# Optimization experiments

Hardware: AMD Instinct MI355X
Metric: run time of the kernel (lower is better)

## Reference

```python
import jax, jax.numpy as jnp
import numpy as np

HID = 64   # basis_hidden_dim
NB = 8     # num_learnable_bases
N = 16     # n_super_nodes
D = 4      # latent_dim
B = 2048   # batch

_PNAMES = ["W1", "b1", "W2", "b2", "W3", "b3", "scale", "aW1", "ab1", "aW2", "ab2", "res"]


def _basis_params(key, din):
    ks = jax.random.split(key, 4)
    s = 0.1
    return [
        jax.random.normal(ks[0], (NB, din, HID)) * s, jnp.zeros((NB, HID)),
        jax.random.normal(ks[1], (NB, HID, HID)) * s, jnp.zeros((NB, HID)),
        jax.random.normal(ks[2], (NB, HID, 1)) * s, jnp.zeros((NB, 1)),
        jnp.ones((NB,)),
        jax.random.normal(ks[3], (din, HID // 2)) * s, jnp.zeros((HID // 2,)),
        jax.random.normal(jax.random.fold_in(ks[3], 1), (HID // 2, NB)) * s, jnp.zeros((NB,)),
        jnp.ones((1,)) * 0.1,
    ]


def setup_inputs() -> dict:
    key = jax.random.key(0)
    k0, k1, k2, k3, k4 = jax.random.split(key, 5)
    inp = {"z_flat": jax.random.normal(k0, (B, N * D), dtype=jnp.float32)}
    for pfx, kk, din in [("pw", k1, 8), ("nd", k2, D), ("gl", k3, N * D)]:
        for nm, v in zip(_PNAMES, _basis_params(kk, din)):
            inp[pfx + "_" + nm] = v
    ks = jax.random.split(k4, 3)
    inp["sel_W1"] = jax.random.normal(ks[0], (N * D, HID)) * 0.1
    inp["sel_b1"] = jnp.zeros((HID,))
    inp["sel_W2"] = jax.random.normal(ks[1], (HID, HID // 2)) * 0.1
    inp["sel_b2"] = jnp.zeros((HID // 2,))
    inp["sel_W3"] = jax.random.normal(ks[2], (HID // 2, 1)) * 0.1
    inp["sel_b3"] = jnp.zeros((1,))
    return inp


def _basis(x, W1, b1, W2, b2, W3, b3, scale, aW1, ab1, aW2, ab2, res):
    # x: [..., din] -> [..., 1]. NB tiny 3-layer MLPs batched over basis axis n.
    h = jax.nn.silu(jnp.einsum('...i,nih->...nh', x, W1) + b1)
    h = jax.nn.silu(jnp.einsum('...nh,nhk->...nk', h, W2) + b2)
    o = (jnp.einsum('...nh,nh->...n', h, W3[..., 0]) + b3[:, 0]) * scale  # [..., NB]
    # attention mixing over the NB basis outputs
    a = jax.nn.silu(x @ aW1 + ab1)
    a = jax.nn.softmax(a @ aW2 + ab2, axis=-1)                            # [..., NB]
    out = jnp.sum(o * a, axis=-1, keepdims=True)
    return out + res * jnp.mean(x, axis=-1, keepdims=True)                # residual


def _forward(z_flat,
             pw_W1, pw_b1, pw_W2, pw_b2, pw_W3, pw_b3, pw_scale, pw_aW1, pw_ab1, pw_aW2, pw_ab2, pw_res,
             nd_W1, nd_b1, nd_W2, nd_b2, nd_W3, nd_b3, nd_scale, nd_aW1, nd_ab1, nd_aW2, nd_ab2, nd_res,
             gl_W1, gl_b1, gl_W2, gl_b2, gl_W3, gl_b3, gl_scale, gl_aW1, gl_ab1, gl_aW2, gl_ab2, gl_res,
             sel_W1, sel_b1, sel_W2, sel_b2, sel_W3, sel_b3):
    b = z_flat.shape[0]
    z_nodes = z_flat.reshape(b, N, D)
    pos = z_nodes[:, :, :2]
    iu, ju = jnp.triu_indices(N, k=1)  # P = N*(N-1)/2 = 120 pairs
    # pairwise distances on upper-triangular pairs (no box wrap: box_size=None)
    diffs = pos[:, iu] - pos[:, ju]                     # [B, P, 2]
    d = jnp.sqrt(jnp.sum(diffs * diffs, axis=-1))       # [B, P]
    d = jnp.maximum(d, 0.001)
    inv_d = 1.0 / (d + 0.1)
    inv_sq = 1.0 / (d * d + 0.1)
    exp_d = jnp.exp(-jnp.minimum(d, 20.0))
    screened = exp_d / (d + 0.1)
    log_d = jnp.log(d + 1.0)
    # learnable pairwise basis: cat(pos_i, vel_i, pos_j, vel_j) == cat(z_i, z_j) for D=4
    pair_in = jnp.concatenate([z_nodes[:, iu], z_nodes[:, ju]], axis=-1)  # [B, P, 8]
    pw = _basis(pair_in, pw_W1, pw_b1, pw_W2, pw_b2, pw_W3, pw_b3, pw_scale,
                pw_aW1, pw_ab1, pw_aW2, pw_ab2, pw_res)[..., 0]           # [B, P]
    nd = _basis(z_nodes, nd_W1, nd_b1, nd_W2, nd_b2, nd_W3, nd_b3, nd_scale,
                nd_aW1, nd_ab1, nd_aW2, nd_ab2, nd_res)[..., 0]           # [B, N]
    gl = _basis(z_flat, gl_W1, gl_b1, gl_W2, gl_b2, gl_W3, gl_b3, gl_scale,
                gl_aW1, gl_ab1, gl_aW2, gl_ab2, gl_res)                   # [B, 1]
    X = jnp.concatenate([z_flat, d, inv_d, inv_sq, exp_d, screened, log_d, pw, nd, gl], axis=1)
    # adaptive feature selection gate
    s = jax.nn.silu(z_flat @ sel_W1 + sel_b1)
    s = jax.nn.silu(s @ sel_W2 + sel_b2)
    s = jax.nn.sigmoid(s @ sel_W3 + sel_b3)             # [B, 1]
    X = X * s
    return jnp.clip(X, -1e6, 1e6)


def reference(z_flat,
              pw_W1, pw_b1, pw_W2, pw_b2, pw_W3, pw_b3, pw_scale, pw_aW1, pw_ab1, pw_aW2, pw_ab2, pw_res,
              nd_W1, nd_b1, nd_W2, nd_b2, nd_W3, nd_b3, nd_scale, nd_aW1, nd_ab1, nd_aW2, nd_ab2, nd_res,
              gl_W1, gl_b1, gl_W2, gl_b2, gl_W3, gl_b3, gl_scale, gl_aW1, gl_ab1, gl_aW2, gl_ab2, gl_res,
              sel_W1, sel_b1, sel_W2, sel_b2, sel_W3, sel_b3):
    return _forward(z_flat,
                    pw_W1, pw_b1, pw_W2, pw_b2, pw_W3, pw_b3, pw_scale, pw_aW1, pw_ab1, pw_aW2, pw_ab2, pw_res,
                    nd_W1, nd_b1, nd_W2, nd_b2, nd_W3, nd_b3, nd_scale, nd_aW1, nd_ab1, nd_aW2, nd_ab2, nd_res,
                    gl_W1, gl_b1, gl_W2, gl_b2, gl_W3, gl_b3, gl_scale, gl_aW1, gl_ab1, gl_aW2, gl_ab2, gl_res,
                    sel_W1, sel_b1, sel_W2, sel_b2, sel_W3, sel_b3)
```

## Files before the change

kernel.cpp:

```cpp
#include <hip/hip_runtime.h>
#include <hip/hip_bf16.h>
#include <math.h>

#define XCOLS 921
#define COL_Z 0
#define COL_D 64
#define COL_INVD 184
#define COL_INVSQ 304
#define COL_EXPD 424
#define COL_SCR 544
#define COL_LOGD 664
#define COL_PW 784
#define COL_ND 904
#define COL_GL 920

#define BATCH 2048
#define NPAIRS 120
#define RPW (BATCH * NPAIRS)
#define RND (BATCH * 16)
#define RGL BATCH
#define RTOT (RPW + RND + RGL)

#define ROWS_BLK 128
#define TILES 8
#define GL_BLK 16
#define PW_BLK 1920
#define ND_BLK 256

#define PREP_SG   512
#define PREP_ROW  1096
#define PREP_WP   128

#define WS_SGATE   0u
#define WS_ZERO    8192u
#define WS_ONE     8448u
#define WS_BW3_PW  8704u
#define WS_BW3_ND  12800u
#define WS_BW3_GL  16896u
#define WS_B1D_GL  20992u
#define WS_W1T_PW  23040u
#define WS_W1T_ND  39424u
#define WS_W1T_GL  55808u
#define WS_W2T_PW  121344u
#define WS_W2T_ND  186880u
#define WS_W2T_GL  252416u
#define WS_XF      317952u
#define WS_XGL     4774400u
#define WS_ATT     5036544u
#define WS_TAIL    14014976u

typedef unsigned short ushort_t;
typedef unsigned int uint_t;
typedef __attribute__((ext_vector_type(8))) short bf16x8;
typedef __attribute__((ext_vector_type(4))) float f32x4;

__device__ __forceinline__ float fast_rcp(float x) { return __builtin_amdgcn_rcpf(x); }
__device__ __forceinline__ float silu_f(float x) { return x * fast_rcp(1.0f + __expf(-x)); }
__device__ __forceinline__ ushort_t f2b(float f) {
    __hip_bfloat16 h = __float2bfloat16(f);
    return __builtin_bit_cast(ushort_t, h);
}
__device__ __forceinline__ uint_t pk2(float a, float b) {
    return (uint_t)f2b(a) | ((uint_t)f2b(b) << 16);
}
__device__ __forceinline__ int permS(int m) {
    return ((m >> 2) & 3) * 8 + (m & 3) + ((m >> 4) & 1) * 4 + ((m >> 5) & 1) * 32;
}

struct AArgs { const float *aW1, *ab1, *aW2, *ab2, *b3, *scale, *res; };
struct PArgs { const float *W1, *b1, *W2, *b2, *W3; };
struct SArgs { const float *W1, *b1, *W2, *b2, *W3, *b3; };

__global__ __launch_bounds__(256) void prep_all_kernel(
    const float* __restrict__ z,
    SArgs sel,
    AArgs apw, AArgs anda, AArgs agl,
    PArgs ppw, PArgs pnd, PArgs pgl,
    char* __restrict__ ws, float* __restrict__ out)
{
    const int bid = blockIdx.x;
    const int tid = threadIdx.x;

    if (bid < PREP_SG) {
        __shared__ float zs[4][64];
        __shared__ float h1[4][64];
        __shared__ float h2s[4][32];
        __shared__ float sgv[4];
        const int grp = tid >> 6, tl = tid & 63;
        const int b = bid * 4 + grp;
        zs[grp][tl] = z[b * 64 + tl];
        __syncthreads();
        {
            float acc = sel.b1[tl];
            #pragma unroll
            for (int i = 0; i < 64; ++i) acc += zs[grp][i] * sel.W1[i * 64 + tl];
            h1[grp][tl] = silu_f(acc);
        }
        __syncthreads();
        if (tl < 32) {
            float acc = sel.b2[tl];
            #pragma unroll
            for (int i = 0; i < 64; ++i) acc += h1[grp][i] * sel.W2[i * 32 + tl];
            h2s[grp][tl] = silu_f(acc);
        }
        __syncthreads();
        if (tl == 0) {
            float acc = sel.b3[0];
            #pragma unroll
            for (int i = 0; i < 32; ++i) acc += h2s[grp][i] * sel.W3[i];
            float s = fast_rcp(1.0f + __expf(-acc));
            sgv[grp] = s;
            ((float*)(ws + WS_SGATE))[b] = s;
        }
        __syncthreads();
        float s = sgv[grp];
        float* row = out + (size_t)b * XCOLS;
        {
            float v = zs[grp][tl] * s;
            row[COL_Z + tl] = fminf(fmaxf(v, -1e6f), 1e6f);
        }
        #pragma unroll
        for (int rep = 0; rep < 2; ++rep) {
            int p = tl + rep * 64;
            if (p < NPAIRS) {
                int i = 0, pp = p;
                while (pp >= 15 - i) { pp -= 15 - i; ++i; }
                int j = i + 1 + pp;
                float dx = zs[grp][i * 4 + 0] - zs[grp][j * 4 + 0];
                float dy = zs[grp][i * 4 + 1] - zs[grp][j * 4 + 1];
                float d = sqrtf(dx * dx + dy * dy);
                d = fmaxf(d, 0.001f);
                float inv_d = fast_rcp(d + 0.1f);
                float inv_sq = fast_rcp(d * d + 0.1f);
                float exp_d = __expf(-fminf(d, 20.0f));
                float screened = exp_d * inv_d;
                float log_d = __logf(d + 1.0f);
                row[COL_D + p] = d * s;
                row[COL_INVD + p] = inv_d * s;
                row[COL_INVSQ + p] = inv_sq * s;
                row[COL_EXPD + p] = exp_d * s;
                row[COL_SCR + p] = screened * s;
                row[COL_LOGD + p] = log_d * s;
            }
        }
        return;
    }

    if (bid >= PREP_SG + PREP_ROW) {
        int t0 = (bid - (PREP_SG + PREP_ROW)) * 256 + tid;
        const int STR = PREP_WP * 256;
        if (t0 < 64) ((float*)(ws + WS_ZERO))[t0] = 0.f;
        if (t0 < 8) ((ushort_t*)(ws + WS_ONE))[t0] = (t0 == 0) ? f2b(1.0f) : (ushort_t)0;
        for (int t = t0; t < 16384; t += STR) {
            int which = t >> 13, u = t & 8191;
            int nn = u >> 10, m = (u >> 4) & 63, k = u & 15;
            int sm = permS(m);
            float v;
            if (which == 0)
                v = (k < 8) ? ppw.W1[nn * 512 + k * 64 + sm]
                  : (k == 8 ? ppw.b1[nn * 64 + sm] : 0.f);
            else
                v = (k < 4) ? pnd.W1[nn * 256 + k * 64 + sm]
                  : (k == 8 ? pnd.b1[nn * 64 + sm] : 0.f);
            ((ushort_t*)(ws + (which == 0 ? WS_W1T_PW : WS_W1T_ND)))[u] = f2b(v);
        }
        for (int t = t0; t < 32768; t += STR) {
            int nn = t >> 12, m = (t >> 6) & 63, k = t & 63;
            ((ushort_t*)(ws + WS_W1T_GL))[t] = f2b(pgl.W1[nn * 4096 + k * 64 + permS(m)]);
        }
        for (int t = t0; t < 512; t += STR) {
            int nn = t >> 6, m = t & 63;
            ((float*)(ws + WS_B1D_GL))[t] = pgl.b1[nn * 64 + permS(m)];
        }
        for (int t = t0; t < 3 * 32768; t += STR) {
            int which = t >> 15, u = t & 32767;
            int nn = u >> 12, kb = (u >> 9) & 7, col = (u >> 3) & 63, e = u & 7;
            int k = (kb & 3) * 8 + e + ((kb >> 2) << 5);
            const float* src = which == 0 ? ppw.W2 : which == 1 ? pnd.W2 : pgl.W2;
            ushort_t* dst = (ushort_t*)(ws + (which == 0 ? WS_W2T_PW : which == 1 ? WS_W2T_ND : WS_W2T_GL));
            dst[u] = f2b(src[nn * 4096 + k * 64 + col]);
        }
        for (int t = t0; t < 1536; t += STR) {
            int which = t >> 9, u = t & 511;
            const float* b2 = which == 0 ? ppw.b2 : which == 1 ? pnd.b2 : pgl.b2;
            const float* W3 = which == 0 ? ppw.W3 : which == 1 ? pnd.W3 : pgl.W3;
            float2* dst = (float2*)(ws + (which == 0 ? WS_BW3_PW : which == 1 ? WS_BW3_ND : WS_BW3_GL));
            dst[u] = make_float2(b2[u], W3[u]);
        }
        return;
    }

    const int urow = (bid - PREP_SG) * 256 + tid;
    float a1acc[32];
    float mean;
    AArgs A;

    if (urow < RPW) {
        A = apw;
        int b = urow / 120, p = urow - b * 120;
        int i = 0, pp = p;
        while (pp >= 15 - i) { pp -= 15 - i; ++i; }
        int j = i + 1 + pp;
        const float* zb = z + b * 64;
        float4 xa = *(const float4*)(zb + i * 4);
        float4 xb = *(const float4*)(zb + j * 4);
        float x[8] = {xa.x, xa.y, xa.z, xa.w, xb.x, xb.y, xb.z, xb.w};
        uint4 xw = make_uint4(pk2(x[0], x[1]), pk2(x[2], x[3]), pk2(x[4], x[5]), pk2(x[6], x[7]));
        *(uint4*)(ws + WS_XF + (size_t)urow * 16) = xw;
        mean = (x[0] + x[1] + x[2] + x[3] + x[4] + x[5] + x[6] + x[7]) * 0.125f;
        #pragma unroll
        for (int u = 0; u < 32; ++u) {
            float acc = A.ab1[u];
            #pragma unroll
            for (int q = 0; q < 8; ++q) acc += x[q] * A.aW1[q * 32 + u];
            a1acc[u] = acc;
        }
    } else if (urow < RPW + RND) {
        A = anda;
        int loc = urow - RPW;
        int b = loc >> 4, node = loc & 15;
        float4 xa = *(const float4*)(z + b * 64 + node * 4);
        float x[4] = {xa.x, xa.y, xa.z, xa.w};
        uint4 xw = make_uint4(pk2(x[0], x[1]), pk2(x[2], x[3]), 0u, 0u);
        *(uint4*)(ws + WS_XF + (size_t)urow * 16) = xw;
        mean = (x[0] + x[1] + x[2] + x[3]) * 0.25f;
        #pragma unroll
        for (int u = 0; u < 32; ++u) {
            float acc = A.ab1[u];
            #pragma unroll
            for (int q = 0; q < 4; ++q) acc += x[q] * A.aW1[q * 32 + u];
            a1acc[u] = acc;
        }
    } else {
        A = agl;
        int r = urow - (RPW + RND);
        const float* zr = z + (size_t)r * 64;
        #pragma unroll
        for (int u = 0; u < 32; ++u) a1acc[u] = A.ab1[u];
        float mn = 0.f;
        #pragma unroll
        for (int c = 0; c < 8; ++c) {
            float4 f0 = *(const float4*)(zr + c * 8);
            float4 f1 = *(const float4*)(zr + c * 8 + 4);
            float xs[8] = {f0.x, f0.y, f0.z, f0.w, f1.x, f1.y, f1.z, f1.w};
            uint4 xw = make_uint4(pk2(xs[0], xs[1]), pk2(xs[2], xs[3]),
                                  pk2(xs[4], xs[5]), pk2(xs[6], xs[7]));
            *(uint4*)(ws + WS_XGL + (size_t)r * 128 + c * 16) = xw;
            #pragma unroll
            for (int q = 0; q < 8; ++q) {
                mn += xs[q];
                float xk = xs[q];
                #pragma unroll
                for (int u = 0; u < 32; ++u) a1acc[u] += xk * A.aW1[(c * 8 + q) * 32 + u];
            }
        }
        mean = mn * (1.0f / 64.0f);
    }

    float lg[8];
    #pragma unroll
    for (int n = 0; n < 8; ++n) lg[n] = A.ab2[n];
    #pragma unroll
    for (int u = 0; u < 32; ++u) {
        float a1 = silu_f(a1acc[u]);
        #pragma unroll
        for (int n = 0; n < 8; ++n) lg[n] += a1 * A.aW2[u * 8 + n];
    }
    float m = lg[0];
    #pragma unroll
    for (int n = 1; n < 8; ++n) m = fmaxf(m, lg[n]);
    float sum = 0.f;
    #pragma unroll
    for (int n = 0; n < 8; ++n) { lg[n] = __expf(lg[n] - m); sum += lg[n]; }
    float inv = fast_rcp(sum);
    float tail = 0.f;
    float as_[8];
    #pragma unroll
    for (int n = 0; n < 8; ++n) {
        float a_n = lg[n] * inv * A.scale[n];
        tail += a_n * A.b3[n];
        as_[n] = a_n;
    }
    float* ag = (float*)(ws + WS_ATT) + (size_t)urow * 8;
    *(float4*)(ag + 0) = make_float4(as_[0], as_[1], as_[2], as_[3]);
    *(float4*)(ag + 4) = make_float4(as_[4], as_[5], as_[6], as_[7]);
    ((float*)(ws + WS_TAIL))[urow] = tail + A.res[0] * mean;
}

__global__ __launch_bounds__(512, 4) void basis_main_kernel(
    const char* __restrict__ ws, float* __restrict__ out)
{
    __shared__ float Att[ROWS_BLK * 9];
    __shared__ float Part[8][ROWS_BLK];
    const int tid = threadIdx.x;
    const int lane = tid & 63;
    const int n = tid >> 6;
    const int g = lane >> 4;
    const int lo = lane & 15;

    const int bid = blockIdx.x;
    int fam, rowbase, ubase;
    uint_t w1t_off, w2t_off, bw3_off;
    if (bid < GL_BLK) {
        fam = 2; rowbase = bid * ROWS_BLK; ubase = RPW + RND + rowbase;
        w1t_off = WS_W1T_GL; w2t_off = WS_W2T_GL; bw3_off = WS_BW3_GL;
    } else if (bid < GL_BLK + PW_BLK) {
        fam = 0; rowbase = (bid - GL_BLK) * ROWS_BLK; ubase = rowbase;
        w1t_off = WS_W1T_PW; w2t_off = WS_W2T_PW; bw3_off = WS_BW3_PW;
    } else {
        fam = 1; rowbase = (bid - (GL_BLK + PW_BLK)) * ROWS_BLK; ubase = RPW + rowbase;
        w1t_off = WS_W1T_ND; w2t_off = WS_W2T_ND; bw3_off = WS_BW3_ND;
    }

    int st_bb = 0, st_colo = 0;
    float st_s = 0.f;
    if (tid < ROWS_BLK) {
        int rg = rowbase + tid;
        if (fam == 0) { st_bb = rg / 120; st_colo = COL_PW + (rg - st_bb * 120); }
        else if (fam == 1) { st_bb = rg >> 4; st_colo = COL_ND + (rg & 15); }
        else { st_bb = rg; st_colo = COL_GL; }
        st_s = ((const float*)(ws + WS_SGATE))[st_bb];
    }

    {
        const float* ag = (const float*)(ws + WS_ATT) + (size_t)ubase * 8;
        #pragma unroll
        for (int q = 0; q < 2; ++q) {
            int idx = tid + q * 512;
            Att[(idx >> 3) * 9 + (idx & 7)] = ag[idx];
        }
        if (tid < ROWS_BLK) Att[tid * 9 + 8] = ((const float*)(ws + WS_TAIL))[ubase + tid];
    }

    const char* w2base = ws + w2t_off + (uint_t)(n * 8192 + g * 1024 + lo * 16);
    bf16x8 w2f0[4], w2f1[4];
    #pragma unroll
    for (int cb = 0; cb < 4; ++cb) {
        w2f0[cb] = *(const bf16x8*)(w2base + cb * 256);
        w2f1[cb] = *(const bf16x8*)(w2base + cb * 256 + 4096);
    }
    float2 bw[4];
    #pragma unroll
    for (int cb = 0; cb < 4; ++cb)
        bw[cb] = ((const float2*)(ws + bw3_off))[n * 64 + cb * 16 + lo];

    __syncthreads();

    if (fam != 2) {
        bf16x8 af[4];
        #pragma unroll
        for (int mt = 0; mt < 4; ++mt) {
            uint_t a = (g < 2) ? (w1t_off + (uint_t)(n * 2048 + (mt * 16 + lo) * 32 + g * 16))
                               : WS_ZERO;
            af[mt] = *(const bf16x8*)(ws + a);
        }
        uint_t xoff = (g == 0) ? (WS_XF + (uint_t)(ubase + lo) * 16u)
                    : (g == 1) ? WS_ONE : WS_ZERO;
        bf16x8 xf = *(const bf16x8*)(ws + xoff);
        #pragma unroll 1
        for (int t = 0; t < TILES; ++t) {
            bf16x8 xf_n = xf;
            if (t + 1 < TILES) {
                uint_t xo = (g == 0) ? (WS_XF + (uint_t)(ubase + (t + 1) * 16 + lo) * 16u)
                          : (g == 1) ? WS_ONE : WS_ZERO;
                xf_n = *(const bf16x8*)(ws + xo);
            }
            const f32x4 zr4 = {0.f, 0.f, 0.f, 0.f};
            f32x4 d0 = __builtin_amdgcn_mfma_f32_16x16x32_bf16(af[0], xf, zr4, 0, 0, 0);
            f32x4 d1 = __builtin_amdgcn_mfma_f32_16x16x32_bf16(af[1], xf, zr4, 0, 0, 0);
            f32x4 d2 = __builtin_amdgcn_mfma_f32_16x16x32_bf16(af[2], xf, zr4, 0, 0, 0);
            f32x4 d3 = __builtin_amdgcn_mfma_f32_16x16x32_bf16(af[3], xf, zr4, 0, 0, 0);
            union { bf16x8 v; uint_t u[4]; } A0, A1;
            A0.u[0] = pk2(silu_f(d0[0]), silu_f(d0[1]));
            A0.u[1] = pk2(silu_f(d0[2]), silu_f(d0[3]));
            A0.u[2] = pk2(silu_f(d1[0]), silu_f(d1[1]));
            A0.u[3] = pk2(silu_f(d1[2]), silu_f(d1[3]));
            A1.u[0] = pk2(silu_f(d2[0]), silu_f(d2[1]));
            A1.u[1] = pk2(silu_f(d2[2]), silu_f(d2[3]));
            A1.u[2] = pk2(silu_f(d3[0]), silu_f(d3[1]));
            A1.u[3] = pk2(silu_f(d3[2]), silu_f(d3[3]));
            float pv0 = 0.f, pv1 = 0.f, pv2 = 0.f, pv3 = 0.f;
            #pragma unroll
            for (int cb = 0; cb < 4; ++cb) {
                f32x4 cinit = {bw[cb].x, bw[cb].x, bw[cb].x, bw[cb].x};
                f32x4 acc = __builtin_amdgcn_mfma_f32_16x16x32_bf16(A0.v, w2f0[cb], cinit, 0, 0, 0);
                acc = __builtin_amdgcn_mfma_f32_16x16x32_bf16(A1.v, w2f1[cb], acc, 0, 0, 0);
                pv0 += silu_f(acc[0]) * bw[cb].y;
                pv1 += silu_f(acc[1]) * bw[cb].y;
                pv2 += silu_f(acc[2]) * bw[cb].y;
                pv3 += silu_f(acc[3]) * bw[cb].y;
            }
            float pvv[4] = {pv0, pv1, pv2, pv3};
            #pragma unroll
            for (int r = 0; r < 4; ++r) {
                float v = pvv[r];
                v += __shfl_xor(v, 1);
                v += __shfl_xor(v, 2);
                v += __shfl_xor(v, 4);
                v += __shfl_xor(v, 8);
                if (lo == 0) {
                    int row = t * 16 + g * 4 + r;
                    Part[n][row] = Att[row * 9 + n] * v;
                }
            }
            xf = xf_n;
        }
    } else {
        float4 b1r[4];
        #pragma unroll
        for (int mt = 0; mt < 4; ++mt)
            b1r[mt] = *(const float4*)(ws + WS_B1D_GL + (uint_t)(n * 64 + mt * 16 + g * 4) * 4u);
        const char* w1b = ws + w1t_off + (uint_t)(n * 8192 + g * 16 + lo * 128);
        const char* xg0 = ws + WS_XGL + (size_t)(rowbase + lo) * 128;
        bf16x8 xf0 = *(const bf16x8*)(xg0 + g * 16);
        bf16x8 xf1 = *(const bf16x8*)(xg0 + 64 + g * 16);
        #pragma unroll 1
        for (int t = 0; t < TILES; ++t) {
            bf16x8 xf0n = xf0, xf1n = xf1;
            if (t + 1 < TILES) {
                const char* xg = ws + WS_XGL + (size_t)(rowbase + (t + 1) * 16 + lo) * 128;
                xf0n = *(const bf16x8*)(xg + g * 16);
                xf1n = *(const bf16x8*)(xg + 64 + g * 16);
            }
            const f32x4 zr4 = {0.f, 0.f, 0.f, 0.f};
            f32x4 d0 = __builtin_amdgcn_mfma_f32_16x16x32_bf16(*(const bf16x8*)(w1b + 0), xf0, zr4, 0, 0, 0);
            d0 = __builtin_amdgcn_mfma_f32_16x16x32_bf16(*(const bf16x8*)(w1b + 64), xf1, d0, 0, 0, 0);
            f32x4 d1 = __builtin_amdgcn_mfma_f32_16x16x32_bf16(*(const bf16x8*)(w1b + 2048), xf0, zr4, 0, 0, 0);
            d1 = __builtin_amdgcn_mfma_f32_16x16x32_bf16(*(const bf16x8*)(w1b + 2112), xf1, d1, 0, 0, 0);
            f32x4 d2 = __builtin_amdgcn_mfma_f32_16x16x32_bf16(*(const bf16x8*)(w1b + 4096), xf0, zr4, 0, 0, 0);
            d2 = __builtin_amdgcn_mfma_f32_16x16x32_bf16(*(const bf16x8*)(w1b + 4160), xf1, d2, 0, 0, 0);
            f32x4 d3 = __builtin_amdgcn_mfma_f32_16x16x32_bf16(*(const bf16x8*)(w1b + 6144), xf0, zr4, 0, 0, 0);
            d3 = __builtin_amdgcn_mfma_f32_16x16x32_bf16(*(const bf16x8*)(w1b + 6208), xf1, d3, 0, 0, 0);
            union { bf16x8 v; uint_t u[4]; } A0, A1;
            A0.u[0] = pk2(silu_f(d0[0] + b1r[0].x), silu_f(d0[1] + b1r[0].y));
            A0.u[1] = pk2(silu_f(d0[2] + b1r[0].z), silu_f(d0[3] + b1r[0].w));
            A0.u[2] = pk2(silu_f(d1[0] + b1r[1].x), silu_f(d1[1] + b1r[1].y));
            A0.u[3] = pk2(silu_f(d1[2] + b1r[1].z), silu_f(d1[3] + b1r[1].w));
            A1.u[0] = pk2(silu_f(d2[0] + b1r[2].x), silu_f(d2[1] + b1r[2].y));
            A1.u[1] = pk2(silu_f(d2[2] + b1r[2].z), silu_f(d2[3] + b1r[2].w));
            A1.u[2] = pk2(silu_f(d3[0] + b1r[3].x), silu_f(d3[1] + b1r[3].y));
            A1.u[3] = pk2(silu_f(d3[2] + b1r[3].z), silu_f(d3[3] + b1r[3].w));
            float pv0 = 0.f, pv1 = 0.f, pv2 = 0.f, pv3 = 0.f;
            #pragma unroll
            for (int cb = 0; cb < 4; ++cb) {
                f32x4 cinit = {bw[cb].x, bw[cb].x, bw[cb].x, bw[cb].x};
                f32x4 acc = __builtin_amdgcn_mfma_f32_16x16x32_bf16(A0.v, w2f0[cb], cinit, 0, 0, 0);
                acc = __builtin_amdgcn_mfma_f32_16x16x32_bf16(A1.v, w2f1[cb], acc, 0, 0, 0);
                pv0 += silu_f(acc[0]) * bw[cb].y;
                pv1 += silu_f(acc[1]) * bw[cb].y;
                pv2 += silu_f(acc[2]) * bw[cb].y;
                pv3 += silu_f(acc[3]) * bw[cb].y;
            }
            float pvv[4] = {pv0, pv1, pv2, pv3};
            #pragma unroll
            for (int r = 0; r < 4; ++r) {
                float v = pvv[r];
                v += __shfl_xor(v, 1);
                v += __shfl_xor(v, 2);
                v += __shfl_xor(v, 4);
                v += __shfl_xor(v, 8);
                if (lo == 0) {
                    int row = t * 16 + g * 4 + r;
                    Part[n][row] = Att[row * 9 + n] * v;
                }
            }
            xf0 = xf0n; xf1 = xf1n;
        }
    }

    __syncthreads();

    if (tid < ROWS_BLK) {
        float v = Att[tid * 9 + 8];
        #pragma unroll
        for (int w = 0; w < 8; ++w) v += Part[w][tid];
        v *= st_s;
        v = fminf(fmaxf(v, -1e6f), 1e6f);
        out[(size_t)st_bb * XCOLS + st_colo] = v;
    }
}

extern "C" void kernel_launch(void* const* d_in, const int* in_sizes, int n_in,
                              void* d_out, int out_size, void* d_ws, size_t ws_size,
                              hipStream_t stream) {
    const float* z = (const float*)d_in[0];
    const float* pw[12]; const float* nd[12]; const float* gl[12];
    for (int i = 0; i < 12; ++i) pw[i] = (const float*)d_in[1 + i];
    for (int i = 0; i < 12; ++i) nd[i] = (const float*)d_in[13 + i];
    for (int i = 0; i < 12; ++i) gl[i] = (const float*)d_in[25 + i];

    SArgs sel = {(const float*)d_in[37], (const float*)d_in[38], (const float*)d_in[39],
                 (const float*)d_in[40], (const float*)d_in[41], (const float*)d_in[42]};

    float* out = (float*)d_out;
    char* ws = (char*)d_ws;

    AArgs apw = {pw[7], pw[8], pw[9], pw[10], pw[5], pw[6], pw[11]};
    AArgs anda = {nd[7], nd[8], nd[9], nd[10], nd[5], nd[6], nd[11]};
    AArgs agl = {gl[7], gl[8], gl[9], gl[10], gl[5], gl[6], gl[11]};
    PArgs ppw = {pw[0], pw[1], pw[2], pw[3], pw[4]};
    PArgs pnd = {nd[0], nd[1], nd[2], nd[3], nd[4]};
    PArgs pgl = {gl[0], gl[1], gl[2], gl[3], gl[4]};

    prep_all_kernel<<<PREP_SG + PREP_ROW + PREP_WP, 256, 0, stream>>>(
        z, sel, apw, anda, agl, ppw, pnd, pgl, ws, out);

    basis_main_kernel<<<GL_BLK + PW_BLK + ND_BLK, 512, 0, stream>>>(ws, out);
}
```

Measured before the change: 128.8 us.

## Halve block to 256 threads, loop waves over two basis passes, use K16 MFMA

The main kernel now launches 256-thread blocks, and each wave handles two basis MLPs in sequence instead of one wave per basis. For the pairwise and node families the first layer uses the 16x16x16 bf16 MFMA when the builtin exists, which removes the half-zero padding of the K32 instruction. The software prefetch of the next x tile is dropped. The aim is less waste in the first layer and a different occupancy balance, at the cost of twice the per-wave serial work and weight reloads per pass.

```diff
diff --git a/kernel.cpp b/kernel.cpp
--- a/kernel.cpp
+++ b/kernel.cpp
@@ -52,7 +52,14 @@
 typedef unsigned short ushort_t;
 typedef unsigned int uint_t;
 typedef __attribute__((ext_vector_type(8))) short bf16x8;
+typedef __attribute__((ext_vector_type(4))) short bf16x4;
 typedef __attribute__((ext_vector_type(4))) float f32x4;
+
+#ifdef __has_builtin
+#if __has_builtin(__builtin_amdgcn_mfma_f32_16x16x16bf16_1k)
+#define HAVE_MFMA16 1
+#endif
+#endif
 
 __device__ __forceinline__ float fast_rcp(float x) { return __builtin_amdgcn_rcpf(x); }
 __device__ __forceinline__ float silu_f(float x) { return x * fast_rcp(1.0f + __expf(-x)); }
@@ -287,14 +294,14 @@
     ((float*)(ws + WS_TAIL))[urow] = tail + A.res[0] * mean;
 }
 
-__global__ __launch_bounds__(512, 4) void basis_main_kernel(
+__global__ __launch_bounds__(256, 5) void basis_main_kernel(
     const char* __restrict__ ws, float* __restrict__ out)
 {
     __shared__ float Att[ROWS_BLK * 9];
     __shared__ float Part[8][ROWS_BLK];
     const int tid = threadIdx.x;
     const int lane = tid & 63;
-    const int n = tid >> 6;
+    const int wave = tid >> 6;
     const int g = lane >> 4;
     const int lo = lane & 15;
 
@@ -325,146 +332,156 @@
     {
         const float* ag = (const float*)(ws + WS_ATT) + (size_t)ubase * 8;
         #pragma unroll
-        for (int q = 0; q < 2; ++q) {
-            int idx = tid + q * 512;
+        for (int q = 0; q < 4; ++q) {
+            int idx = tid + q * 256;
             Att[(idx >> 3) * 9 + (idx & 7)] = ag[idx];
         }
         if (tid < ROWS_BLK) Att[tid * 9 + 8] = ((const float*)(ws + WS_TAIL))[ubase + tid];
     }
-
-    const char* w2base = ws + w2t_off + (uint_t)(n * 8192 + g * 1024 + lo * 16);
-    bf16x8 w2f0[4], w2f1[4];
-    #pragma unroll
-    for (int cb = 0; cb < 4; ++cb) {
-        w2f0[cb] = *(const bf16x8*)(w2base + cb * 256);
-        w2f1[cb] = *(const bf16x8*)(w2base + cb * 256 + 4096);
-    }
-    float2 bw[4];
-    #pragma unroll
-    for (int cb = 0; cb < 4; ++cb)
-        bw[cb] = ((const float2*)(ws + bw3_off))[n * 64 + cb * 16 + lo];
-
     __syncthreads();
 
-    if (fam != 2) {
-        bf16x8 af[4];
-        #pragma unroll
-        for (int mt = 0; mt < 4; ++mt) {
-            uint_t a = (g < 2) ? (w1t_off + (uint_t)(n * 2048 + (mt * 16 + lo) * 32 + g * 16))
-                               : WS_ZERO;
-            af[mt] = *(const bf16x8*)(ws + a);
-        }
-        uint_t xoff = (g == 0) ? (WS_XF + (uint_t)(ubase + lo) * 16u)
-                    : (g == 1) ? WS_ONE : WS_ZERO;
-        bf16x8 xf = *(const bf16x8*)(ws + xoff);
-        #pragma unroll 1
-        for (int t = 0; t < TILES; ++t) {
-            bf16x8 xf_n = xf;
-            if (t + 1 < TILES) {
-                uint_t xo = (g == 0) ? (WS_XF + (uint_t)(ubase + (t + 1) * 16 + lo) * 16u)
-                          : (g == 1) ? WS_ONE : WS_ZERO;
-                xf_n = *(const bf16x8*)(ws + xo);
+    #pragma unroll 1
+    for (int pass = 0; pass < 2; ++pass) {
+        const int n = wave + pass * 4;
+
+        const char* w2base = ws + w2t_off + (uint_t)(n * 8192 + g * 1024 + lo * 16);
+        bf16x8 w2f0[4], w2f1[4];
+        #pragma unroll
+        for (int cb = 0; cb < 4; ++cb) {
+            w2f0[cb] = *(const bf16x8*)(w2base + cb * 256);
+            w2f1[cb] = *(const bf16x8*)(w2base + cb * 256 + 4096);
+        }
+        float2 bw[4];
+        #pragma unroll
+        for (int cb = 0; cb < 4; ++cb)
+            bw[cb] = ((const float2*)(ws + bw3_off))[n * 64 + cb * 16 + lo];
+
+        if (fam != 2) {
+#ifdef HAVE_MFMA16
+            bf16x4 af[4];
+            #pragma unroll
+            for (int mt = 0; mt < 4; ++mt)
+                af[mt] = *(const bf16x4*)(ws + w1t_off +
+                        (uint_t)(n * 2048 + (mt * 16 + lo) * 32 + g * 8));
+            const uint_t xcon = (g == 2) ? WS_ONE : WS_ZERO;
+            #pragma unroll 1
+            for (int t = 0; t < TILES; ++t) {
+                uint_t xoff = (g < 2)
+                    ? (WS_XF + (uint_t)(ubase + t * 16 + lo) * 16u + (uint_t)(g * 8))
+                    : xcon;
+                bf16x4 xf = *(const bf16x4*)(ws + xoff);
+                const f32x4 zr4 = {0.f, 0.f, 0.f, 0.f};
+                f32x4 d0 = __builtin_amdgcn_mfma_f32_16x16x16bf16_1k(af[0], xf, zr4, 0, 0, 0);
+                f32x4 d1 = __builtin_amdgcn_mfma_f32_16x16x16bf16_1k(af[1], xf, zr4, 0, 0, 0);
+                f32x4 d2 = __builtin_amdgcn_mfma_f32_16x16x16bf16_1k(af[2], xf, zr4, 0, 0, 0);
+                f32x4 d3 = __builtin_amdgcn_mfma_f32_16x16x16bf16_1k(af[3], xf, zr4, 0, 0, 0);
+#else
+            bf16x8 af[4];
+            #pragma unroll
+            for (int mt = 0; mt < 4; ++mt) {
+                uint_t a = (g < 2) ? (w1t_off + (uint_t)(n * 2048 + (mt * 16 + lo) * 32 + g * 16))
+                                   : WS_ZERO;
+                af[mt] = *(const bf16x8*)(ws + a);
             }
-            const f32x4 zr4 = {0.f, 0.f, 0.f, 0.f};
-            f32x4 d0 = __builtin_amdgcn_mfma_f32_16x16x32_bf16(af[0], xf, zr4, 0, 0, 0);
-            f32x4 d1 = __builtin_amdgcn_mfma_f32_16x16x32_bf16(af[1], xf, zr4, 0, 0, 0);
-            f32x4 d2 = __builtin_amdgcn_mfma_f32_16x16x32_bf16(af[2], xf, zr4, 0, 0, 0);
-            f32x4 d3 = __builtin_amdgcn_mfma_f32_16x16x32_bf16(af[3], xf, zr4, 0, 0, 0);
-            union { bf16x8 v; uint_t u[4]; } A0, A1;
-            A0.u[0] = pk2(silu_f(d0[0]), silu_f(d0[1]));
-            A0.u[1] = pk2(silu_f(d0[2]), silu_f(d0[3]));
-            A0.u[2] = pk2(silu_f(d1[0]), silu_f(d1[1]));
-            A0.u[3] = pk2(silu_f(d1[2]), silu_f(d1[3]));
-            A1.u[0] = pk2(silu_f(d2[0]), silu_f(d2[1]));
-            A1.u[1] = pk2(silu_f(d2[2]), silu_f(d2[3]));
-            A1.u[2] = pk2(silu_f(d3[0]), silu_f(d3[1]));
-            A1.u[3] = pk2(silu_f(d3[2]), silu_f(d3[3]));
-            float pv0 = 0.f, pv1 = 0.f, pv2 = 0.f, pv3 = 0.f;
-            #pragma unroll
-            for (int cb = 0; cb < 4; ++cb) {
-                f32x4 cinit = {bw[cb].x, bw[cb].x, bw[cb].x, bw[cb].x};
-                f32x4 acc = __builtin_amdgcn_mfma_f32_16x16x32_bf16(A0.v, w2f0[cb], cinit, 0, 0, 0);
-                acc = __builtin_amdgcn_mfma_f32_16x16x32_bf16(A1.v, w2f1[cb], acc, 0, 0, 0);
-                pv0 += silu_f(acc[0]) * bw[cb].y;
-                pv1 += silu_f(acc[1]) * bw[cb].y;
-                pv2 += silu_f(acc[2]) * bw[cb].y;
-                pv3 += silu_f(acc[3]) * bw[cb].y;
-            }
-            float pvv[4] = {pv0, pv1, pv2, pv3};
-            #pragma unroll
-            for (int r = 0; r < 4; ++r) {
-                float v = pvv[r];
-                v += __shfl_xor(v, 1);
-                v += __shfl_xor(v, 2);
-                v += __shfl_xor(v, 4);
-                v += __shfl_xor(v, 8);
-                if (lo == 0) {
-                    int row = t * 16 + g * 4 + r;
-                    Part[n][row] = Att[row * 9 + n] * v;
+            #pragma unroll 1
+            for (int t = 0; t < TILES; ++t) {
+                uint_t xoff = (g == 0) ? (WS_XF + (uint_t)(ubase + t * 16 + lo) * 16u)
+                            : (g == 1) ? WS_ONE : WS_ZERO;
+                bf16x8 xf = *(const bf16x8*)(ws + xoff);
+                const f32x4 zr4 = {0.f, 0.f, 0.f, 0.f};
+                f32x4 d0 = __builtin_amdgcn_mfma_f32_16x16x32_bf16(af[0], xf, zr4, 0, 0, 0);
+                f32x4 d1 = __builtin_amdgcn_mfma_f32_16x16x32_bf16(af[1], xf, zr4, 0, 0, 0);
+                f32x4 d2 = __builtin_amdgcn_mfma_f32_16x16x32_bf16(af[2], xf, zr4, 0, 0, 0);
+                f32x4 d3 = __builtin_amdgcn_mfma_f32_16x16x32_bf16(af[3], xf, zr4, 0, 0, 0);
+#endif
+                union { bf16x8 v; uint_t u[4]; } A0, A1;
+                A0.u[0] = pk2(silu_f(d0[0]), silu_f(d0[1]));
+                A0.u[1] = pk2(silu_f(d0[2]), silu_f(d0[3]));
+                A0.u[2] = pk2(silu_f(d1[0]), silu_f(d1[1]));
+                A0.u[3] = pk2(silu_f(d1[2]), silu_f(d1[3]));
+                A1.u[0] = pk2(silu_f(d2[0]), silu_f(d2[1]));
+                A1.u[1] = pk2(silu_f(d2[2]), silu_f(d2[3]));
+                A1.u[2] = pk2(silu_f(d3[0]), silu_f(d3[1]));
+                A1.u[3] = pk2(silu_f(d3[2]), silu_f(d3[3]));
+                float pv0 = 0.f, pv1 = 0.f, pv2 = 0.f, pv3 = 0.f;
+                #pragma unroll
+                for (int cb = 0; cb < 4; ++cb) {
+                    f32x4 cinit = {bw[cb].x, bw[cb].x, bw[cb].x, bw[cb].x};
+                    f32x4 acc = __builtin_amdgcn_mfma_f32_16x16x32_bf16(A0.v, w2f0[cb], cinit, 0, 0, 0);
+                    acc = __builtin_amdgcn_mfma_f32_16x16x32_bf16(A1.v, w2f1[cb], acc, 0, 0, 0);
+                    pv0 += silu_f(acc[0]) * bw[cb].y;
+                    pv1 += silu_f(acc[1]) * bw[cb].y;
+                    pv2 += silu_f(acc[2]) * bw[cb].y;
+                    pv3 += silu_f(acc[3]) * bw[cb].y;
+                }
+                float pvv[4] = {pv0, pv1, pv2, pv3};
+                #pragma unroll
+                for (int r = 0; r < 4; ++r) {
+                    float v = pvv[r];
+                    v += __shfl_xor(v, 1);
+                    v += __shfl_xor(v, 2);
+                    v += __shfl_xor(v, 4);
+                    v += __shfl_xor(v, 8);
+                    if (lo == 0) {
+                        int row = t * 16 + g * 4 + r;
+                        Part[n][row] = Att[row * 9 + n] * v;
+                    }
                 }
             }
-            xf = xf_n;
-        }
-    } else {
-        float4 b1r[4];
-        #pragma unroll
-        for (int mt = 0; mt < 4; ++mt)
-            b1r[mt] = *(const float4*)(ws + WS_B1D_GL + (uint_t)(n * 64 + mt * 16 + g * 4) * 4u);
-        const char* w1b = ws + w1t_off + (uint_t)(n * 8192 + g * 16 + lo * 128);
-        const char* xg0 = ws + WS_XGL + (size_t)(rowbase + lo) * 128;
-        bf16x8 xf0 = *(const bf16x8*)(xg0 + g * 16);
-        bf16x8 xf1 = *(const bf16x8*)(xg0 + 64 + g * 16);
-        #pragma unroll 1
-        for (int t = 0; t < TILES; ++t) {
-            bf16x8 xf0n = xf0, xf1n = xf1;
-            if (t + 1 < TILES) {
-                const char* xg = ws + WS_XGL + (size_t)(rowbase + (t + 1) * 16 + lo) * 128;
-                xf0n = *(const bf16x8*)(xg + g * 16);
-                xf1n = *(const bf16x8*)(xg + 64 + g * 16);
-            }
-            const f32x4 zr4 = {0.f, 0.f, 0.f, 0.f};
-            f32x4 d0 = __builtin_amdgcn_mfma_f32_16x16x32_bf16(*(const bf16x8*)(w1b + 0), xf0, zr4, 0, 0, 0);
-            d0 = __builtin_amdgcn_mfma_f32_16x16x32_bf16(*(const bf16x8*)(w1b + 64), xf1, d0, 0, 0, 0);
-            f32x4 d1 = __builtin_amdgcn_mfma_f32_16x16x32_bf16(*(const bf16x8*)(w1b + 2048), xf0, zr4, 0, 0, 0);
-            d1 = __builtin_amdgcn_mfma_f32_16x16x32_bf16(*(const bf16x8*)(w1b + 2112), xf1, d1, 0, 0, 0);
-            f32x4 d2 = __builtin_amdgcn_mfma_f32_16x16x32_bf16(*(const bf16x8*)(w1b + 4096), xf0, zr4, 0, 0, 0);
-            d2 = __builtin_amdgcn_mfma_f32_16x16x32_bf16(*(const bf16x8*)(w1b + 4160), xf1, d2, 0, 0, 0);
-            f32x4 d3 = __builtin_amdgcn_mfma_f32_16x16x32_bf16(*(const bf16x8*)(w1b + 6144), xf0, zr4, 0, 0, 0);
-            d3 = __builtin_amdgcn_mfma_f32_16x16x32_bf16(*(const bf16x8*)(w1b + 6208), xf1, d3, 0, 0, 0);
-            union { bf16x8 v; uint_t u[4]; } A0, A1;
-            A0.u[0] = pk2(silu_f(d0[0] + b1r[0].x), silu_f(d0[1] + b1r[0].y));
-            A0.u[1] = pk2(silu_f(d0[2] + b1r[0].z), silu_f(d0[3] + b1r[0].w));
-            A0.u[2] = pk2(silu_f(d1[0] + b1r[1].x), silu_f(d1[1] + b1r[1].y));
-            A0.u[3] = pk2(silu_f(d1[2] + b1r[1].z), silu_f(d1[3] + b1r[1].w));
-            A1.u[0] = pk2(silu_f(d2[0] + b1r[2].x), silu_f(d2[1] + b1r[2].y));
-            A1.u[1] = pk2(silu_f(d2[2] + b1r[2].z), silu_f(d2[3] + b1r[2].w));
-            A1.u[2] = pk2(silu_f(d3[0] + b1r[3].x), silu_f(d3[1] + b1r[3].y));
-            A1.u[3] = pk2(silu_f(d3[2] + b1r[3].z), silu_f(d3[3] + b1r[3].w));
-            float pv0 = 0.f, pv1 = 0.f, pv2 = 0.f, pv3 = 0.f;
-            #pragma unroll
-            for (int cb = 0; cb < 4; ++cb) {
-                f32x4 cinit = {bw[cb].x, bw[cb].x, bw[cb].x, bw[cb].x};
-                f32x4 acc = __builtin_amdgcn_mfma_f32_16x16x32_bf16(A0.v, w2f0[cb], cinit, 0, 0, 0);
-                acc = __builtin_amdgcn_mfma_f32_16x16x32_bf16(A1.v, w2f1[cb], acc, 0, 0, 0);
-                pv0 += silu_f(acc[0]) * bw[cb].y;
-                pv1 += silu_f(acc[1]) * bw[cb].y;
-                pv2 += silu_f(acc[2]) * bw[cb].y;
-                pv3 += silu_f(acc[3]) * bw[cb].y;
-            }
-            float pvv[4] = {pv0, pv1, pv2, pv3};
-            #pragma unroll
-            for (int r = 0; r < 4; ++r) {
-                float v = pvv[r];
-                v += __shfl_xor(v, 1);
-                v += __shfl_xor(v, 2);
-                v += __shfl_xor(v, 4);
-                v += __shfl_xor(v, 8);
-                if (lo == 0) {
-                    int row = t * 16 + g * 4 + r;
-                    Part[n][row] = Att[row * 9 + n] * v;
+        } else {
+            float4 b1r[4];
+            #pragma unroll
+            for (int mt = 0; mt < 4; ++mt)
+                b1r[mt] = *(const float4*)(ws + WS_B1D_GL + (uint_t)(n * 64 + mt * 16 + g * 4) * 4u);
+            const char* w1b = ws + w1t_off + (uint_t)(n * 8192 + g * 16 + lo * 128);
+            #pragma unroll 1
+            for (int t = 0; t < TILES; ++t) {
+                const char* xg = ws + WS_XGL + (size_t)(rowbase + t * 16 + lo) * 128;
+                bf16x8 xf0 = *(const bf16x8*)(xg + g * 16);
+                bf16x8 xf1 = *(const bf16x8*)(xg + 64 + g * 16);
+                const f32x4 zr4 = {0.f, 0.f, 0.f, 0.f};
+                f32x4 d0 = __builtin_amdgcn_mfma_f32_16x16x32_bf16(*(const bf16x8*)(w1b + 0), xf0, zr4, 0, 0, 0);
+                d0 = __builtin_amdgcn_mfma_f32_16x16x32_bf16(*(const bf16x8*)(w1b + 64), xf1, d0, 0, 0, 0);
+                f32x4 d1 = __builtin_amdgcn_mfma_f32_16x16x32_bf16(*(const bf16x8*)(w1b + 2048), xf0, zr4, 0, 0, 0);
+                d1 = __builtin_amdgcn_mfma_f32_16x16x32_bf16(*(const bf16x8*)(w1b + 2112), xf1, d1, 0, 0, 0);
+                f32x4 d2 = __builtin_amdgcn_mfma_f32_16x16x32_bf16(*(const bf16x8*)(w1b + 4096), xf0, zr4, 0, 0, 0);
+                d2 = __builtin_amdgcn_mfma_f32_16x16x32_bf16(*(const bf16x8*)(w1b + 4160), xf1, d2, 0, 0, 0);
+                f32x4 d3 = __builtin_amdgcn_mfma_f32_16x16x32_bf16(*(const bf16x8*)(w1b + 6144), xf0, zr4, 0, 0, 0);
+                d3 = __builtin_amdgcn_mfma_f32_16x16x32_bf16(*(const bf16x8*)(w1b + 6208), xf1, d3, 0, 0, 0);
+                union { bf16x8 v; uint_t u[4]; } A0, A1;
+                A0.u[0] = pk2(silu_f(d0[0] + b1r[0].x), silu_f(d0[1] + b1r[0].y));
+                A0.u[1] = pk2(silu_f(d0[2] + b1r[0].z), silu_f(d0[3] + b1r[0].w));
+                A0.u[2] = pk2(silu_f(d1[0] + b1r[1].x), silu_f(d1[1] + b1r[1].y));
+                A0.u[3] = pk2(silu_f(d1[2] + b1r[1].z), silu_f(d1[3] + b1r[1].w));
+                A1.u[0] = pk2(silu_f(d2[0] + b1r[2].x), silu_f(d2[1] + b1r[2].y));
+                A1.u[1] = pk2(silu_f(d2[2] + b1r[2].z), silu_f(d2[3] + b1r[2].w));
+                A1.u[2] = pk2(silu_f(d3[0] + b1r[3].x), silu_f(d3[1] + b1r[3].y));
+                A1.u[3] = pk2(silu_f(d3[2] + b1r[3].z), silu_f(d3[3] + b1r[3].w));
+                float pv0 = 0.f, pv1 = 0.f, pv2 = 0.f, pv3 = 0.f;
+                #pragma unroll
+                for (int cb = 0; cb < 4; ++cb) {
+                    f32x4 cinit = {bw[cb].x, bw[cb].x, bw[cb].x, bw[cb].x};
+                    f32x4 acc = __builtin_amdgcn_mfma_f32_16x16x32_bf16(A0.v, w2f0[cb], cinit, 0, 0, 0);
+                    acc = __builtin_amdgcn_mfma_f32_16x16x32_bf16(A1.v, w2f1[cb], acc, 0, 0, 0);
+                    pv0 += silu_f(acc[0]) * bw[cb].y;
+                    pv1 += silu_f(acc[1]) * bw[cb].y;
+                    pv2 += silu_f(acc[2]) * bw[cb].y;
+                    pv3 += silu_f(acc[3]) * bw[cb].y;
+                }
+                float pvv[4] = {pv0, pv1, pv2, pv3};
+                #pragma unroll
+                for (int r = 0; r < 4; ++r) {
+                    float v = pvv[r];
+                    v += __shfl_xor(v, 1);
+                    v += __shfl_xor(v, 2);
+                    v += __shfl_xor(v, 4);
+                    v += __shfl_xor(v, 8);
+                    if (lo == 0) {
+                        int row = t * 16 + g * 4 + r;
+                        Part[n][row] = Att[row * 9 + n] * v;
+                    }
                 }
             }
-            xf0 = xf0n; xf1 = xf1n;
         }
     }
 
@@ -505,5 +522,5 @@
     prep_all_kernel<<<PREP_SG + PREP_ROW + PREP_WP, 256, 0, stream>>>(
         z, sel, apw, anda, agl, ppw, pnd, pgl, ws, out);
 
-    basis_main_kernel<<<GL_BLK + PW_BLK + ND_BLK, 512, 0, stream>>>(ws, out);
+    basis_main_kernel<<<GL_BLK + PW_BLK + ND_BLK, 256, 0, stream>>>(ws, out);
 }
```

New measurement: 175.0 us. 1.36x slower.
